# Kernel optimization log

Hardware: AMD Instinct MI355X
Metric: run time of the kernel (lower is better)

Reference implementation:

```python
import jax, jax.numpy as jnp
import numpy as np

FFT_LEN = 512
FFT_BINS = FFT_LEN // 2 + 1  # 257


def _dft_kernels(fft_len):
    n = np.arange(fft_len)
    k = np.arange(fft_len // 2 + 1).reshape(-1, 1)
    ang = 2.0 * np.pi * k * n / fft_len
    real_kernel = jnp.asarray(np.cos(ang), dtype=jnp.float32)   # (bins, fft_len)
    imag_kernel = jnp.asarray(-np.sin(ang), dtype=jnp.float32)  # (bins, fft_len)
    return real_kernel, imag_kernel


def setup_inputs() -> dict:
    key = jax.random.key(0)
    x = jax.random.normal(key, (16, 4000, FFT_LEN), dtype=jnp.float32)
    real_kernel, imag_kernel = _dft_kernels(FFT_LEN)
    return {"x": x, "real_kernel": real_kernel, "imag_kernel": imag_kernel}


def reference(x, real_kernel, imag_kernel):
    # x: (B, F, N); kernels: (K, N) with K = N//2 + 1
    B, F, _ = x.shape
    real = jnp.einsum("bfn,kn->bfk", x, real_kernel)  # (B, F, K)
    imag = jnp.einsum("bfn,kn->bfk", x, imag_kernel)  # (B, F, K)
    # interleave real/imag per frequency bin: [..., r0, i0, r1, i1, ...]
    out = jnp.stack([real, imag], axis=-1).reshape(B, F, -1)  # (B, F, 2K)
    return out
```

## Files before the change

kernel.cpp:

```cpp
#include <hip/hip_runtime.h>

typedef _Float16 f16x8 __attribute__((ext_vector_type(8)));
typedef float f32x4 __attribute__((ext_vector_type(4)));

#define MDIM 64000
#define KDIM 512
#define NCOLS 514
#define NPAD 512
#define BM 128
#define BN 128
#define BK 32
#define KT (KDIM / BK)
#define NT 4
#define NWG 2000

#define GLOAD_LDS16(g, l)                                        \
  __builtin_amdgcn_global_load_lds(                              \
      (const __attribute__((address_space(1))) void*)(g),        \
      (__attribute__((address_space(3))) void*)(l), 16, 0, 0)

__global__ void prep_w(const float* __restrict__ rk, const float* __restrict__ ik,
                       _Float16* __restrict__ wb) {
  int n = blockIdx.x;
  int k = threadIdx.x;
  int bin = n >> 1;
  const float* src = (n & 1) ? ik : rk;
  wb[(size_t)n * KDIM + k] = (_Float16)src[bin * KDIM + k];
}

__global__ __launch_bounds__(256, 4)
void dft_gemm(const float* __restrict__ x, const _Float16* __restrict__ wb,
              float* __restrict__ out) {
  __shared__ float As[BM * BK];
  __shared__ _Float16 Bs[BN * BK];

  const int tid = threadIdx.x;
  const int l   = tid & 63;
  const int w   = tid >> 6;
  const int lr  = l & 15;
  const int lg  = l >> 4;
  const int wm  = (w >> 1) * 64;
  const int wn  = (w & 1) * 64;

  const int wgid = (blockIdx.x & 7) * (NWG / 8) + (blockIdx.x >> 3);
  const int mt = wgid >> 2;
  const int nt = wgid & 3;
  const int m0 = mt * BM;
  const int n0 = nt * BN;

  f32x4 acc[4][4] = {};
  float nyq = 0.0f;

  const int arow0 = w * 32 + (l >> 3);
  const float* asrc = x + (size_t)(m0 + arow0) * KDIM + (((l & 7) ^ (l >> 3)) << 2);

  const int brow0 = w * 32 + (l >> 2);
  const _Float16* bsrc =
      wb + (size_t)(n0 + brow0) * KDIM + (((l & 3) ^ ((l >> 3) & 3)) << 3);

  for (int kt = 0; kt < KT; ++kt) {
    if (kt) __syncthreads();

#pragma unroll
    for (int s = 0; s < 4; ++s)
      GLOAD_LDS16(asrc + (size_t)s * 8 * KDIM + kt * BK,
                  &As[(w * 32 + s * 8) * BK]);
#pragma unroll
    for (int s = 0; s < 2; ++s)
      GLOAD_LDS16(bsrc + (size_t)s * 16 * KDIM + kt * BK,
                  &Bs[(w * 32 + s * 16) * BK]);
    __syncthreads();

    {
      f16x8 av[4], bv[4];
#pragma unroll
      for (int fm = 0; fm < 4; ++fm) {
        int row = wm + fm * 16 + lr;
        int sw  = lr & 7;
        int c0  = lg * 2;
        f32x4 lo = *reinterpret_cast<const f32x4*>(&As[row * BK + ((c0 ^ sw) << 2)]);
        f32x4 hi = *reinterpret_cast<const f32x4*>(&As[row * BK + (((c0 + 1) ^ sw) << 2)]);
        f16x8 h;
        h[0] = (_Float16)lo[0]; h[1] = (_Float16)lo[1];
        h[2] = (_Float16)lo[2]; h[3] = (_Float16)lo[3];
        h[4] = (_Float16)hi[0]; h[5] = (_Float16)hi[1];
        h[6] = (_Float16)hi[2]; h[7] = (_Float16)hi[3];
        av[fm] = h;
      }
#pragma unroll
      for (int fn = 0; fn < 4; ++fn) {
        int row = wn + fn * 16 + lr;
        int c   = lg ^ ((lr >> 1) & 3);
        bv[fn] = *reinterpret_cast<const f16x8*>(&Bs[row * BK + (c << 3)]);
      }
#pragma unroll
      for (int fm = 0; fm < 4; ++fm)
#pragma unroll
        for (int fn = 0; fn < 4; ++fn)
          acc[fm][fn] = __builtin_amdgcn_mfma_f32_16x16x32_f16(
              av[fm], bv[fn], acc[fm][fn], 0, 0, 0);
    }

    if (nt == 0) {
      const int nrow = tid >> 1;
#pragma unroll
      for (int j = 0; j < 4; ++j) {
        int c = ((tid & 1) * 4 + j) ^ (nrow & 7);
        f32x4 v = *reinterpret_cast<const f32x4*>(&As[nrow * BK + (c << 2)]);
        nyq += (v[0] - v[1]) + (v[2] - v[3]);
      }
    }
  }

#pragma unroll
  for (int fm = 0; fm < 4; ++fm) {
#pragma unroll
    for (int rr = 0; rr < 4; ++rr) {
      int row = m0 + wm + fm * 16 + lg * 4 + rr;
      size_t base = (size_t)row * NCOLS;
#pragma unroll
      for (int fn = 0; fn < 4; ++fn)
        out[base + n0 + wn + fn * 16 + lr] = acc[fm][fn][rr];
    }
  }

  if (nt == 0) {
    float tot = nyq + __shfl_xor(nyq, 1);
    if ((tid & 1) == 0) {
      size_t base = (size_t)(m0 + (tid >> 1)) * NCOLS;
      out[base + 512] = tot;
      out[base + 513] = 0.0f;
    }
  }
}

extern "C" void kernel_launch(void* const* d_in, const int* in_sizes, int n_in,
                              void* d_out, int out_size, void* d_ws, size_t ws_size,
                              hipStream_t stream) {
  const float* x  = (const float*)d_in[0];
  const float* rk = (const float*)d_in[1];
  const float* ik = (const float*)d_in[2];
  float* out = (float*)d_out;
  _Float16* wb = (_Float16*)d_ws;

  prep_w<<<dim3(NPAD), dim3(KDIM), 0, stream>>>(rk, ik, wb);

  dim3 grid(NWG);
  dft_gemm<<<grid, dim3(256), 0, stream>>>(x, wb, out);
}
```

Before: 82.97 us.

## Preload full weight panel into LDS and stream x directly from global into registers

Restructures the GEMM so each workgroup of 512 threads loads a 64-column slice of the fp16 weights for the full K=512 into LDS once, then streams x rows straight from global memory into registers with no per-K-step LDS staging or barriers. Tile shape changes from 128x128 to 256x64 with 8 waves, each owning 32 rows. The Nyquist bin is now computed from the register-resident x values and reduced with lane shuffles. This removes the 16 barrier-synchronised LDS round trips per tile. In exchange, x is re-read from global by 8 column tiles instead of 4, and the unbuffered direct global loads may expose latency.

```diff
diff --git a/kernel.cpp b/kernel.cpp
--- a/kernel.cpp
+++ b/kernel.cpp
@@ -4,14 +4,12 @@
 typedef float f32x4 __attribute__((ext_vector_type(4)));
 
 #define MDIM 64000
-#define KDIM 512
+#define KD 512
 #define NCOLS 514
-#define NPAD 512
-#define BM 128
-#define BN 128
-#define BK 32
-#define KT (KDIM / BK)
-#define NT 4
+#define BM 256
+#define BN 64
+#define KT 16
+#define NT 8
 #define NWG 2000
 
 #define GLOAD_LDS16(g, l)                                        \
@@ -25,111 +23,91 @@
   int k = threadIdx.x;
   int bin = n >> 1;
   const float* src = (n & 1) ? ik : rk;
-  wb[(size_t)n * KDIM + k] = (_Float16)src[bin * KDIM + k];
+  wb[(size_t)n * KD + k] = (_Float16)src[bin * KD + k];
 }
 
-__global__ __launch_bounds__(256, 4)
+__global__ __launch_bounds__(512, 3)
 void dft_gemm(const float* __restrict__ x, const _Float16* __restrict__ wb,
               float* __restrict__ out) {
-  __shared__ float As[BM * BK];
-  __shared__ _Float16 Bs[BN * BK];
+  __shared__ _Float16 Bp[BN * KD];
 
   const int tid = threadIdx.x;
-  const int l   = tid & 63;
-  const int w   = tid >> 6;
-  const int lr  = l & 15;
-  const int lg  = l >> 4;
-  const int wm  = (w >> 1) * 64;
-  const int wn  = (w & 1) * 64;
+  const int l  = tid & 63;
+  const int w  = tid >> 6;
+  const int lr = l & 15;
+  const int lg = l >> 4;
 
   const int wgid = (blockIdx.x & 7) * (NWG / 8) + (blockIdx.x >> 3);
-  const int mt = wgid >> 2;
-  const int nt = wgid & 3;
-  const int m0 = mt * BM;
-  const int n0 = nt * BN;
-
-  f32x4 acc[4][4] = {};
-  float nyq = 0.0f;
-
-  const int arow0 = w * 32 + (l >> 3);
-  const float* asrc = x + (size_t)(m0 + arow0) * KDIM + (((l & 7) ^ (l >> 3)) << 2);
-
-  const int brow0 = w * 32 + (l >> 2);
-  const _Float16* bsrc =
-      wb + (size_t)(n0 + brow0) * KDIM + (((l & 3) ^ ((l >> 3) & 3)) << 3);
-
-  for (int kt = 0; kt < KT; ++kt) {
-    if (kt) __syncthreads();
+  const int mt = wgid >> 3, nt = wgid & 7;
+  const int m0 = mt * BM, n0 = nt * BN;
 
 #pragma unroll
-    for (int s = 0; s < 4; ++s)
-      GLOAD_LDS16(asrc + (size_t)s * 8 * KDIM + kt * BK,
-                  &As[(w * 32 + s * 8) * BK]);
+  for (int s = 0; s < 8; ++s) {
+    int row = w * 8 + s;
+    int cl  = l ^ (row & 7);
+    GLOAD_LDS16(wb + (size_t)(n0 + row) * KD + cl * 8, &Bp[row * KD]);
+  }
+  __syncthreads();
+
+  f32x4 acc[2][4] = {};
+  float nyq[2] = {0.0f, 0.0f};
+  const bool donyq = (nt == 0);
+
+  const float* a0 = x + (size_t)(m0 + w * 32 + lr) * KD + lg * 8;
+
 #pragma unroll
-    for (int s = 0; s < 2; ++s)
-      GLOAD_LDS16(bsrc + (size_t)s * 16 * KDIM + kt * BK,
-                  &Bs[(w * 32 + s * 16) * BK]);
-    __syncthreads();
+  for (int kt = 0; kt < KT; ++kt) {
+    f16x8 av[2], bv[4];
+#pragma unroll
+    for (int fm = 0; fm < 2; ++fm) {
+      f32x4 lo = *reinterpret_cast<const f32x4*>(a0 + (size_t)fm * 16 * KD + kt * 32);
+      f32x4 hi = *reinterpret_cast<const f32x4*>(a0 + (size_t)fm * 16 * KD + kt * 32 + 4);
+      f16x8 h;
+      h[0] = (_Float16)lo[0]; h[1] = (_Float16)lo[1];
+      h[2] = (_Float16)lo[2]; h[3] = (_Float16)lo[3];
+      h[4] = (_Float16)hi[0]; h[5] = (_Float16)hi[1];
+      h[6] = (_Float16)hi[2]; h[7] = (_Float16)hi[3];
+      av[fm] = h;
+      if (donyq)
+        nyq[fm] += (lo[0] - lo[1]) + (lo[2] - lo[3]) + (hi[0] - hi[1]) + (hi[2] - hi[3]);
+    }
+#pragma unroll
+    for (int fn = 0; fn < 4; ++fn) {
+      int row = fn * 16 + lr;
+      int pc  = (kt * 4 + lg) ^ (row & 7);
+      bv[fn] = *reinterpret_cast<const f16x8*>(&Bp[row * KD + pc * 8]);
+    }
+#pragma unroll
+    for (int fm = 0; fm < 2; ++fm)
+#pragma unroll
+      for (int fn = 0; fn < 4; ++fn)
+        acc[fm][fn] = __builtin_amdgcn_mfma_f32_16x16x32_f16(
+            av[fm], bv[fn], acc[fm][fn], 0, 0, 0);
+  }
 
-    {
-      f16x8 av[4], bv[4];
 #pragma unroll
-      for (int fm = 0; fm < 4; ++fm) {
-        int row = wm + fm * 16 + lr;
-        int sw  = lr & 7;
-        int c0  = lg * 2;
-        f32x4 lo = *reinterpret_cast<const f32x4*>(&As[row * BK + ((c0 ^ sw) << 2)]);
-        f32x4 hi = *reinterpret_cast<const f32x4*>(&As[row * BK + (((c0 + 1) ^ sw) << 2)]);
-        f16x8 h;
-        h[0] = (_Float16)lo[0]; h[1] = (_Float16)lo[1];
-        h[2] = (_Float16)lo[2]; h[3] = (_Float16)lo[3];
-        h[4] = (_Float16)hi[0]; h[5] = (_Float16)hi[1];
-        h[6] = (_Float16)hi[2]; h[7] = (_Float16)hi[3];
-        av[fm] = h;
-      }
+  for (int fm = 0; fm < 2; ++fm) {
 #pragma unroll
-      for (int fn = 0; fn < 4; ++fn) {
-        int row = wn + fn * 16 + lr;
-        int c   = lg ^ ((lr >> 1) & 3);
-        bv[fn] = *reinterpret_cast<const f16x8*>(&Bs[row * BK + (c << 3)]);
-      }
+    for (int rr = 0; rr < 4; ++rr) {
+      int row = m0 + w * 32 + fm * 16 + lg * 4 + rr;
+      size_t base = (size_t)row * NCOLS;
 #pragma unroll
-      for (int fm = 0; fm < 4; ++fm)
-#pragma unroll
-        for (int fn = 0; fn < 4; ++fn)
-          acc[fm][fn] = __builtin_amdgcn_mfma_f32_16x16x32_f16(
-              av[fm], bv[fn], acc[fm][fn], 0, 0, 0);
-    }
-
-    if (nt == 0) {
-      const int nrow = tid >> 1;
-#pragma unroll
-      for (int j = 0; j < 4; ++j) {
-        int c = ((tid & 1) * 4 + j) ^ (nrow & 7);
-        f32x4 v = *reinterpret_cast<const f32x4*>(&As[nrow * BK + (c << 2)]);
-        nyq += (v[0] - v[1]) + (v[2] - v[3]);
-      }
+      for (int fn = 0; fn < 4; ++fn)
+        out[base + n0 + fn * 16 + lr] = acc[fm][fn][rr];
     }
   }
 
+  if (donyq) {
 #pragma unroll
-  for (int fm = 0; fm < 4; ++fm) {
-#pragma unroll
-    for (int rr = 0; rr < 4; ++rr) {
-      int row = m0 + wm + fm * 16 + lg * 4 + rr;
-      size_t base = (size_t)row * NCOLS;
-#pragma unroll
-      for (int fn = 0; fn < 4; ++fn)
-        out[base + n0 + wn + fn * 16 + lr] = acc[fm][fn][rr];
-    }
-  }
-
-  if (nt == 0) {
-    float tot = nyq + __shfl_xor(nyq, 1);
-    if ((tid & 1) == 0) {
-      size_t base = (size_t)(m0 + (tid >> 1)) * NCOLS;
-      out[base + 512] = tot;
-      out[base + 513] = 0.0f;
+    for (int fm = 0; fm < 2; ++fm) {
+      float t = nyq[fm];
+      t += __shfl_xor(t, 16);
+      t += __shfl_xor(t, 32);
+      if (lg == 0) {
+        size_t base = (size_t)(m0 + w * 32 + fm * 16 + lr) * NCOLS;
+        out[base + 512] = t;
+        out[base + 513] = 0.0f;
+      }
     }
   }
 }
@@ -143,8 +121,8 @@
   float* out = (float*)d_out;
   _Float16* wb = (_Float16*)d_ws;
 
-  prep_w<<<dim3(NPAD), dim3(KDIM), 0, stream>>>(rk, ik, wb);
+  prep_w<<<dim3(KD), dim3(KD), 0, stream>>>(rk, ik, wb);
 
   dim3 grid(NWG);
-  dft_gemm<<<grid, dim3(256), 0, stream>>>(x, wb, out);
+  dft_gemm<<<grid, dim3(512), 0, stream>>>(x, wb, out);
 }
```

Measured after the change: 143.3 us. 72.7% more time.
